# Performance work log

Hardware: AMD Instinct MI355X
Metric: run time of the kernel (lower is better)

Reference implementation:

```python
import jax, jax.numpy as jnp
import numpy as np

K = 16          # nsample
EPS = 1e-5      # BatchNorm eps
NEG_SLOPE = 0.1 # LeakyReLU slope


def _knn_gather(pc2, pc1, feat2, k):
    """pc2 [B,N2,3], pc1 [B,N1,3], feat2 [B,N2,C] ->
       neighbor_xyz [B,N1,k,3], neighbor_feat [B,N1,k,C] (k nearest in pc2 per pc1 point)."""
    # squared euclidean distances (monotone in cdist, same topk indices)
    d2 = (jnp.sum(pc1 * pc1, -1)[:, :, None]
          - 2.0 * jnp.einsum('bic,bjc->bij', pc1, pc2)
          + jnp.sum(pc2 * pc2, -1)[:, None, :])
    idx = jax.lax.top_k(-d2, k)[1]            # [B,N1,k] smallest distances
    gather = jax.vmap(lambda pts, i: pts[i])  # batch-wise fancy gather
    return gather(pc2, idx), gather(feat2, idx)


def _weightnet(xyz, W1, b1, gamma, beta, mean, var, W2, b2):
    """xyz [B,N,K,3] -> [B,N,K,C_out]; Conv2d(1x1)->BN(eval)->ReLU->Conv2d(1x1)."""
    h = jnp.einsum('bnkc,oc->bnko', xyz, W1) + b1
    h = gamma * (h - mean) * jax.lax.rsqrt(var + EPS) + beta
    h = jax.nn.relu(h)
    return jnp.einsum('bnkc,oc->bnko', h, W2) + b2


def _correlator(pc1, pc2, feature1, feature2, mlp_params, wn1, wn2):
    pc1_t = pc1.transpose(0, 2, 1)   # [B,N,3]
    pc2_t = pc2.transpose(0, 2, 1)
    f1 = feature1.transpose(0, 2, 1) # [B,N,C]
    f2 = feature2.transpose(0, 2, 1)
    # Stage 1: point-to-patch cost volume
    nbr_xyz, nbr_f2 = _knn_gather(pc2_t, pc1_t, f2, K)
    direction = nbr_xyz - pc1_t[:, :, None, :]                     # [B,N,K,3]
    f1e = jnp.broadcast_to(f1[:, :, None, :], nbr_f2.shape[:3] + (f1.shape[-1],))
    x = jnp.concatenate([f1e, nbr_f2, direction], axis=-1)         # [B,N,K,2C+3]
    for W, b in mlp_params:
        x = jax.nn.leaky_relu(jnp.einsum('bnkc,oc->bnko', x, W) + b, NEG_SLOPE)
    w1 = _weightnet(direction, *wn1)
    x = jnp.sum(w1 * x, axis=2)                                    # [B,N,C]
    # Stage 2: patch-to-patch self aggregation in pc1 space
    nbr_xyz2, nbr_self = _knn_gather(pc1_t, pc1_t, x, K)
    direction2 = nbr_xyz2 - pc1_t[:, :, None, :]
    w2 = _weightnet(direction2, *wn2)
    out = jnp.sum(w2 * nbr_self, axis=2)                           # [B,N,C]
    return out.transpose(0, 2, 1)                                  # [B,C,N]


def setup_inputs() -> dict:
    key = jax.random.key(0)
    ks = jax.random.split(key, 24)
    B, N, C = 2, 4096, 256
    inc = 2 * C + 3  # 515
    nrm = lambda k, s, sc: (jax.random.normal(k, s, dtype=jnp.float32) * sc)
    uni = lambda k, s: jax.random.uniform(k, s, dtype=jnp.float32, minval=0.5, maxval=1.5)
    return {
        'pc1': nrm(ks[0], (B, 3, N), 1.0),
        'pc2': nrm(ks[1], (B, 3, N), 1.0),
        'feature1': nrm(ks[2], (B, C, N), 1.0),
        'feature2': nrm(ks[3], (B, C, N), 1.0),
        # MLP 1x1 conv stack
        'W0': nrm(ks[4], (C, inc), 0.05), 'b0': jnp.zeros((C,), jnp.float32),
        'W1': nrm(ks[5], (C, C), 0.05),  'b1': jnp.zeros((C,), jnp.float32),
        'W2': nrm(ks[6], (C, C), 0.05),  'b2': jnp.zeros((C,), jnp.float32),
        # WeightNet 1 (3->8->C)
        'wn1_W1': nrm(ks[7], (8, 3), 0.5), 'wn1_b1': jnp.zeros((8,), jnp.float32),
        'wn1_gamma': uni(ks[8], (8,)), 'wn1_beta': nrm(ks[9], (8,), 0.1),
        'wn1_mean': nrm(ks[10], (8,), 0.1), 'wn1_var': uni(ks[11], (8,)),
        'wn1_W2': nrm(ks[12], (C, 8), 0.1), 'wn1_b2': jnp.zeros((C,), jnp.float32),
        # WeightNet 2
        'wn2_W1': nrm(ks[13], (8, 3), 0.5), 'wn2_b1': jnp.zeros((8,), jnp.float32),
        'wn2_gamma': uni(ks[14], (8,)), 'wn2_beta': nrm(ks[15], (8,), 0.1),
        'wn2_mean': nrm(ks[16], (8,), 0.1), 'wn2_var': uni(ks[17], (8,)),
        'wn2_W2': nrm(ks[18], (C, 8), 0.1), 'wn2_b2': jnp.zeros((C,), jnp.float32),
    }


def reference(pc1, pc2, feature1, feature2,
              W0, b0, W1, b1, W2, b2,
              wn1_W1, wn1_b1, wn1_gamma, wn1_beta, wn1_mean, wn1_var, wn1_W2, wn1_b2,
              wn2_W1, wn2_b1, wn2_gamma, wn2_beta, wn2_mean, wn2_var, wn2_W2, wn2_b2):
    mlp_params = [(W0, b0), (W1, b1), (W2, b2)]
    wn1 = (wn1_W1, wn1_b1, wn1_gamma, wn1_beta, wn1_mean, wn1_var, wn1_W2, wn1_b2)
    wn2 = (wn2_W1, wn2_b1, wn2_gamma, wn2_beta, wn2_mean, wn2_var, wn2_W2, wn2_b2)
    return _correlator(pc1, pc2, feature1, feature2, mlp_params, wn1, wn2)
```

## Files before the change

### kernel.cpp

```cpp
#include <hip/hip_runtime.h>
#include <math.h>

#define KNB 16
#define NPTS 4096
#define NB 2
#define CH 256
#define BNEPS 1e-5f

#define MTOT (NB * NPTS * KNB)
#define BM 128

typedef short bf16x8 __attribute__((ext_vector_type(8)));
typedef float f32x4 __attribute__((ext_vector_type(4)));

__device__ __forceinline__ unsigned short f2bf(float x) {
  unsigned u = __float_as_uint(x);
  return (unsigned short)((u + 0x7fffu + ((u >> 16) & 1u)) >> 16);
}
__device__ __forceinline__ float bf2f(unsigned short h) {
  return __uint_as_float(((unsigned)h) << 16);
}

#define GLOAD_LDS16(g, l)                                                     \
  __builtin_amdgcn_global_load_lds(                                           \
      (const __attribute__((address_space(1))) unsigned int*)(g),             \
      (__attribute__((address_space(3))) unsigned int*)(l), 16, 0, 0)

__global__ __launch_bounds__(256) void pack2_pts(const float* __restrict__ pc1,
                                                 const float* __restrict__ pc2,
                                                 float4* __restrict__ pk1,
                                                 float4* __restrict__ pk2) {
  int id = blockIdx.x * 256 + threadIdx.x;
  const float* in = (id < 8192) ? pc1 : pc2;
  float4* out = (id < 8192) ? pk1 : pk2;
  int q = id & 8191;
  int b = q >> 12, n = q & 4095;
  const float* pb = in + (size_t)b * 3 * NPTS;
  float x = pb[n], y = pb[NPTS + n], z = pb[2 * NPTS + n];
  float nn = __fadd_rn(__fadd_rn(__fmul_rn(x, x), __fmul_rn(y, y)), __fmul_rn(z, z));
  out[q] = make_float4(x, y, z, nn);
}

__global__ __launch_bounds__(256) void knn3c_kernel(const float4* __restrict__ pk1,
                                                    const float4* __restrict__ pk2,
                                                    int* __restrict__ idx1,
                                                    int* __restrict__ idx2) {
  __shared__ unsigned short sarr[4][4096];
  __shared__ unsigned long long surv[4][128];
  const int wid = threadIdx.x >> 6;
  const int lane = threadIdx.x & 63;
  const int gw = blockIdx.x * 4 + wid;
  const int which = gw >> 13;
  const int qi = gw & 8191;
  const int b = qi >> 12;
  const float4* pts = (which ? pk1 : pk2) + ((size_t)b << 12);
  float4 qp = pk1[qi];
  const float qx = qp.x, qy = qp.y, qz = qp.z, qn = qp.w;
  unsigned short* S = sarr[wid];

  unsigned int mymin = 0xFFFFu;
#pragma unroll 8
  for (int it = 0; it < 64; ++it) {
    int j = (it << 6) + lane;
    float4 pt = pts[j];
    float dot = __fadd_rn(__fadd_rn(__fmul_rn(qx, pt.x), __fmul_rn(qy, pt.y)),
                          __fmul_rn(qz, pt.z));
    float d = __fadd_rn(__fsub_rn(qn, __fmul_rn(2.f, dot)), pt.w);
    unsigned int u = __float_as_uint(d);
    unsigned int s = u ^ (unsigned int)(((int)u >> 31) | (int)0x80000000);
    unsigned int k16 = s >> 16;
    S[j] = (unsigned short)k16;
    mymin = mymin < k16 ? mymin : k16;
  }

  unsigned int v = mymin;
#pragma unroll
  for (int k = 2; k <= 64; k <<= 1) {
#pragma unroll
    for (int jj = k >> 1; jj >= 1; jj >>= 1) {
      unsigned int o = (unsigned int)__shfl_xor((int)v, jj);
      bool up = ((lane & k) == 0);
      bool low = ((lane & jj) == 0);
      bool tmin = (up == low);
      unsigned int mn = v < o ? v : o;
      unsigned int mx = v < o ? o : v;
      v = tmin ? mn : mx;
    }
  }

  unsigned long long* SV = surv[wid];
  unsigned int thr = (unsigned int)__shfl((int)v, 15);
  int base = 0;
  for (int attempt = 0; attempt < 2; ++attempt) {
    SV[lane] = ~0ull;
    SV[64 + lane] = ~0ull;
    base = 0;
    for (int it = 0; it < 64; ++it) {
      int j = (it << 6) + lane;
      bool hit = (unsigned int)S[j] <= thr;
      unsigned long long m = __ballot(hit);
      if (m) {
        float4 pt = pts[j];
        float dot = __fadd_rn(__fadd_rn(__fmul_rn(qx, pt.x), __fmul_rn(qy, pt.y)),
                              __fmul_rn(qz, pt.z));
        float d = __fadd_rn(__fsub_rn(qn, __fmul_rn(2.f, dot)), pt.w);
        unsigned int u = __float_as_uint(d);
        unsigned int s = u ^ (unsigned int)(((int)u >> 31) | (int)0x80000000);
        int r = base + (int)__popcll(m & ((1ull << lane) - 1ull));
        if (hit && r < 128) SV[r] = ((unsigned long long)s << 32) | (unsigned int)j;
        base += (int)__popcll(m);
      }
    }
    if (base <= 128) break;
    if (attempt == 0) {
      int idx = 23, cnt = 0, tries = 0;
      for (;;) {
        thr = (unsigned int)__shfl((int)v, idx);
        cnt = 0;
        for (int it = 0; it < 64; ++it) {
          unsigned long long m = __ballot((unsigned int)S[(it << 6) + lane] <= thr);
          cnt += __popcll(m);
        }
        if ((cnt >= 16 && cnt <= 128) || ++tries >= 6) break;
        if (cnt < 16) idx = (idx + 12 > 63) ? 63 : idx + 12;
        else idx = (idx - 8 < 0) ? 0 : idx - 8;
      }
    }
  }
  unsigned long long k0 = SV[lane];
  unsigned long long k1 = SV[64 + lane];

#pragma unroll
  for (int k = 2; k <= 128; k <<= 1) {
#pragma unroll
    for (int jj = k >> 1; jj >= 1; jj >>= 1) {
      if (jj == 64) {
        unsigned long long a = k0 < k1 ? k0 : k1;
        unsigned long long c = k0 < k1 ? k1 : k0;
        k0 = a; k1 = c;
      } else {
        {
          unsigned long long o = __shfl_xor(k0, jj);
          bool up = ((lane & k) == 0);
          bool low = ((lane & jj) == 0);
          bool tmin = (up == low);
          unsigned long long mn = k0 < o ? k0 : o;
          unsigned long long mx = k0 < o ? o : k0;
          k0 = tmin ? mn : mx;
        }
        {
          unsigned long long o = __shfl_xor(k1, jj);
          int e = 64 + lane;
          bool up = ((e & k) == 0);
          bool low = ((lane & jj) == 0);
          bool tmin = (up == low);
          unsigned long long mn = k1 < o ? k1 : o;
          unsigned long long mx = k1 < o ? o : k1;
          k1 = tmin ? mn : mx;
        }
      }
    }
  }

  int* op = (which ? idx2 : idx1) + (size_t)qi * KNB;
  if (lane < 16) op[lane] = (int)(k0 & 0xFFFFFFFFu);
}

__global__ __launch_bounds__(256) void conv_feat2(const float* __restrict__ f1,
                                                  const float* __restrict__ f2,
                                                  unsigned short* __restrict__ f1b,
                                                  unsigned short* __restrict__ f2b) {
  int gid = blockIdx.x;
  const float* in = (gid < 8192) ? f1 : f2;
  unsigned short* out = (gid < 8192) ? f1b : f2b;
  int bn = gid & 8191;
  int b = bn >> 12, n = bn & 4095;
  int c = threadIdx.x;
  out[(size_t)bn * CH + c] = f2bf(in[((size_t)(b * CH + c)) * NPTS + n]);
}

__global__ __launch_bounds__(256) void conv_w2(const float* __restrict__ W0,
                                               const float* __restrict__ W1,
                                               const float* __restrict__ W2,
                                               unsigned short* __restrict__ W0a,
                                               unsigned short* __restrict__ W0bp,
                                               unsigned short* __restrict__ W1b,
                                               unsigned short* __restrict__ W2b) {
  int r = blockIdx.x, c = threadIdx.x;
  if (r < 256) {
    W0a[r * 256 + c] = f2bf(W0[(size_t)r * 515 + c]);
    W0bp[r * 256 + c] = f2bf(W0[(size_t)r * 515 + 256 + c]);
  } else if (r < 512) {
    int rr = r - 256;
    W1b[rr * 256 + c] = f2bf(W1[rr * 256 + c]);
  } else {
    int rr = r - 512;
    W2b[rr * 256 + c] = f2bf(W2[rr * 256 + c]);
  }
}

__global__ __launch_bounds__(512) void small_gemm(
    const unsigned short* __restrict__ f1b, const unsigned short* __restrict__ f2b,
    const unsigned short* __restrict__ W0a, const unsigned short* __restrict__ W0bp,
    const float* __restrict__ b0, float* __restrict__ g1, float* __restrict__ G2) {
  __shared__ char smem[8192 + 16384];
  const int tid = threadIdx.x;
  const int lane = tid & 63;
  const int w = tid >> 6;
  const int wm = w >> 2, wn = w & 3;
  const bool isG2 = blockIdx.x >= 64;
  const int m0 = (blockIdx.x & 63) * BM;
  const unsigned short* Asrc = isG2 ? f2b : f1b;
  const unsigned short* Wb = isG2 ? W0bp : W0a;
  float* dst = isG2 ? G2 : g1;

  f32x4 acc[4][4];
#pragma unroll
  for (int nf = 0; nf < 4; ++nf) {
    float bv = isG2 ? 0.f : b0[wn * 64 + nf * 16 + (lane & 15)];
#pragma unroll
    for (int mf = 0; mf < 4; ++mf) acc[mf][nf] = (f32x4){bv, bv, bv, bv};
  }

  const int ar = tid >> 2;
  const int aql = (tid & 3) ^ ((ar >> 1) & 3);
  const int am = m0 + ar;
  const int br0 = tid >> 2;
  const int bq0 = (tid & 3) ^ ((br0 >> 1) & 3);
  const int br1 = (tid + 512) >> 2;
  const int bq1 = (tid & 3) ^ ((br1 >> 1) & 3);

  char* AsW = smem + (w << 10);
  char* BsW0 = smem + 8192 + (w << 10);
  char* BsW1 = smem + 8192 + 8192 + (w << 10);

  for (int kc = 0; kc < 8; ++kc) {
    __syncthreads();
    GLOAD_LDS16(Asrc + ((size_t)am << 8) + kc * 32 + aql * 8, AsW);
    GLOAD_LDS16(Wb + (size_t)br0 * 256 + kc * 32 + bq0 * 8, BsW0);
    GLOAD_LDS16(Wb + (size_t)br1 * 256 + kc * 32 + bq1 * 8, BsW1);
    __syncthreads();

    bf16x8 af[4], bfr[4];
#pragma unroll
    for (int mf = 0; mf < 4; ++mf) {
      int r = wm * 64 + mf * 16 + (lane & 15);
      int off = r * 64 + ((((lane >> 4)) ^ ((r >> 1) & 3)) << 4);
      af[mf] = *(const bf16x8*)(smem + off);
    }
#pragma unroll
    for (int nf = 0; nf < 4; ++nf) {
      int r = wn * 64 + nf * 16 + (lane & 15);
      int off = r * 64 + ((((lane >> 4)) ^ ((r >> 1) & 3)) << 4);
      bfr[nf] = *(const bf16x8*)(smem + 8192 + off);
    }
#pragma unroll
    for (int mf = 0; mf < 4; ++mf)
#pragma unroll
      for (int nf = 0; nf < 4; ++nf)
        acc[mf][nf] = __builtin_amdgcn_mfma_f32_16x16x32_bf16(af[mf], bfr[nf], acc[mf][nf], 0, 0, 0);
  }

#pragma unroll
  for (int mf = 0; mf < 4; ++mf) {
#pragma unroll
    for (int nf = 0; nf < 4; ++nf) {
      int n = wn * 64 + nf * 16 + (lane & 15);
#pragma unroll
      for (int j = 0; j < 4; ++j) {
        int m = m0 + wm * 64 + mf * 16 + (lane >> 4) * 4 + j;
        dst[(size_t)m * 256 + n] = acc[mf][nf][j];
      }
    }
  }
}

__global__ __launch_bounds__(256) void combine_kernel(
    const float* __restrict__ g1, const float* __restrict__ G2,
    const float* __restrict__ W0,
    const float* __restrict__ pc1, const float* __restrict__ pc2,
    const int* __restrict__ idx1,
    const float* __restrict__ wW1, const float* __restrict__ wb1,
    const float* __restrict__ wg, const float* __restrict__ wbe,
    const float* __restrict__ wmn, const float* __restrict__ wv,
    unsigned short* __restrict__ h1, float* __restrict__ h1wn) {
  __shared__ int nbrs[KNB];
  __shared__ float dirs[KNB][4];
  int bn = blockIdx.x;
  int b = bn >> 12, n = bn & 4095;
  int t = threadIdx.x;
  if (t < KNB) nbrs[t] = idx1[(size_t)bn * KNB + t];
  __syncthreads();
  if (t < 128) {
    int k = t >> 3, jj = t & 7;
    int j = nbrs[k];
    const float* p1 = pc1 + (size_t)b * 3 * NPTS;
    const float* p2 = pc2 + (size_t)b * 3 * NPTS;
    float d0 = p2[j] - p1[n];
    float d1 = p2[NPTS + j] - p1[NPTS + n];
    float d2 = p2[2 * NPTS + j] - p1[2 * NPTS + n];
    if (jj == 0) { dirs[k][0] = d0; dirs[k][1] = d1; dirs[k][2] = d2; }
    float hv = wb1[jj];
    hv = fmaf(d0, wW1[jj * 3], hv);
    hv = fmaf(d1, wW1[jj * 3 + 1], hv);
    hv = fmaf(d2, wW1[jj * 3 + 2], hv);
    hv = wg[jj] * (hv - wmn[jj]) * (1.f / sqrtf(wv[jj] + BNEPS)) + wbe[jj];
    h1wn[(size_t)(bn * KNB + k) * 8 + jj] = fmaxf(hv, 0.f);
  }
  __syncthreads();
  int c = t;
  float g1v = g1[((size_t)bn << 8) + c];
  float wc0 = W0[(size_t)c * 515 + 512];
  float wc1 = W0[(size_t)c * 515 + 513];
  float wc2 = W0[(size_t)c * 515 + 514];
  const float* G2b = G2 + (((size_t)b << 12) << 8);
  unsigned short* hp = h1 + ((size_t)bn * KNB) * 256 + c;
#pragma unroll
  for (int k = 0; k < KNB; ++k) {
    float s = g1v + G2b[((size_t)nbrs[k] << 8) + c];
    s = fmaf(dirs[k][0], wc0, s);
    s = fmaf(dirs[k][1], wc1, s);
    s = fmaf(dirs[k][2], wc2, s);
    s = s >= 0.f ? s : 0.1f * s;
    hp[k * 256] = f2bf(s);
  }
}

__global__ __launch_bounds__(512) void gemm256(
    const unsigned short* __restrict__ Asrc, const unsigned short* __restrict__ Wb,
    const float* __restrict__ bias, unsigned short* __restrict__ dst) {
  __shared__ char smem[8192 + 16384];
  const int tid = threadIdx.x;
  const int lane = tid & 63;
  const int w = tid >> 6;
  const int wm = w >> 2, wn = w & 3;
  const int m0 = blockIdx.x * BM;

  f32x4 acc[4][4];
#pragma unroll
  for (int nf = 0; nf < 4; ++nf) {
    float bv = bias[wn * 64 + nf * 16 + (lane & 15)];
#pragma unroll
    for (int mf = 0; mf < 4; ++mf) acc[mf][nf] = (f32x4){bv, bv, bv, bv};
  }

  const int ar = tid >> 2;
  const int aql = (tid & 3) ^ ((ar >> 1) & 3);
  const int am = m0 + ar;
  const int br0 = tid >> 2;
  const int bq0 = (tid & 3) ^ ((br0 >> 1) & 3);
  const int br1 = (tid + 512) >> 2;
  const int bq1 = (tid & 3) ^ ((br1 >> 1) & 3);

  char* AsW = smem + (w << 10);
  char* BsW0 = smem + 8192 + (w << 10);
  char* BsW1 = smem + 8192 + 8192 + (w << 10);

  for (int kc = 0; kc < 8; ++kc) {
    __syncthreads();
    GLOAD_LDS16(Asrc + ((size_t)am << 8) + kc * 32 + aql * 8, AsW);
    GLOAD_LDS16(Wb + (size_t)br0 * 256 + kc * 32 + bq0 * 8, BsW0);
    GLOAD_LDS16(Wb + (size_t)br1 * 256 + kc * 32 + bq1 * 8, BsW1);
    __syncthreads();

    bf16x8 af[4], bfr[4];
#pragma unroll
    for (int mf = 0; mf < 4; ++mf) {
      int r = wm * 64 + mf * 16 + (lane & 15);
      int off = r * 64 + ((((lane >> 4)) ^ ((r >> 1) & 3)) << 4);
      af[mf] = *(const bf16x8*)(smem + off);
    }
#pragma unroll
    for (int nf = 0; nf < 4; ++nf) {
      int r = wn * 64 + nf * 16 + (lane & 15);
      int off = r * 64 + ((((lane >> 4)) ^ ((r >> 1) & 3)) << 4);
      bfr[nf] = *(const bf16x8*)(smem + 8192 + off);
    }
#pragma unroll
    for (int mf = 0; mf < 4; ++mf)
#pragma unroll
      for (int nf = 0; nf < 4; ++nf)
        acc[mf][nf] = __builtin_amdgcn_mfma_f32_16x16x32_bf16(af[mf], bfr[nf], acc[mf][nf], 0, 0, 0);
  }

#pragma unroll
  for (int mf = 0; mf < 4; ++mf) {
#pragma unroll
    for (int nf = 0; nf < 4; ++nf) {
      int n = wn * 64 + nf * 16 + (lane & 15);
#pragma unroll
      for (int j = 0; j < 4; ++j) {
        int m = m0 + wm * 64 + mf * 16 + (lane >> 4) * 4 + j;
        float v = acc[mf][nf][j];
        v = v >= 0.f ? v : 0.1f * v;
        dst[(size_t)m * 256 + n] = f2bf(v);
      }
    }
  }
}

__global__ __launch_bounds__(512) void gemm256_wred(
    const unsigned short* __restrict__ Asrc, const unsigned short* __restrict__ Wb,
    const float* __restrict__ bias, const float* __restrict__ h1wn,
    const float* __restrict__ wW2, const float* __restrict__ wb2,
    float* __restrict__ out1) {
  __shared__ char smem[8192 + 16384];
  __shared__ float hw[1024];
  const int tid = threadIdx.x;
  const int lane = tid & 63;
  const int w = tid >> 6;
  const int wm = w >> 2, wn = w & 3;
  const int m0 = blockIdx.x * BM;

  hw[tid] = h1wn[(size_t)blockIdx.x * 1024 + tid];
  hw[tid + 512] = h1wn[(size_t)blockIdx.x * 1024 + 512 + tid];

  f32x4 acc[4][4];
#pragma unroll
  for (int nf = 0; nf < 4; ++nf) {
    float bv = bias[wn * 64 + nf * 16 + (lane & 15)];
#pragma unroll
    for (int mf = 0; mf < 4; ++mf) acc[mf][nf] = (f32x4){bv, bv, bv, bv};
  }

  const int ar = tid >> 2;
  const int aql = (tid & 3) ^ ((ar >> 1) & 3);
  const int am = m0 + ar;
  const int br0 = tid >> 2;
  const int bq0 = (tid & 3) ^ ((br0 >> 1) & 3);
  const int br1 = (tid + 512) >> 2;
  const int bq1 = (tid & 3) ^ ((br1 >> 1) & 3);

  char* AsW = smem + (w << 10);
  char* BsW0 = smem + 8192 + (w << 10);
  char* BsW1 = smem + 8192 + 8192 + (w << 10);

  for (int kc = 0; kc < 8; ++kc) {
    __syncthreads();
    GLOAD_LDS16(Asrc + ((size_t)am << 8) + kc * 32 + aql * 8, AsW);
    GLOAD_LDS16(Wb + (size_t)br0 * 256 + kc * 32 + bq0 * 8, BsW0);
    GLOAD_LDS16(Wb + (size_t)br1 * 256 + kc * 32 + bq1 * 8, BsW1);
    __syncthreads();

    bf16x8 af[4], bfr[4];
#pragma unroll
    for (int mf = 0; mf < 4; ++mf) {
      int r = wm * 64 + mf * 16 + (lane & 15);
      int off = r * 64 + ((((lane >> 4)) ^ ((r >> 1) & 3)) << 4);
      af[mf] = *(const bf16x8*)(smem + off);
    }
#pragma unroll
    for (int nf = 0; nf < 4; ++nf) {
      int r = wn * 64 + nf * 16 + (lane & 15);
      int off = r * 64 + ((((lane >> 4)) ^ ((r >> 1) & 3)) << 4);
      bfr[nf] = *(const bf16x8*)(smem + 8192 + off);
    }
#pragma unroll
    for (int mf = 0; mf < 4; ++mf)
#pragma unroll
      for (int nf = 0; nf < 4; ++nf)
        acc[mf][nf] = __builtin_amdgcn_mfma_f32_16x16x32_bf16(af[mf], bfr[nf], acc[mf][nf], 0, 0, 0);
  }

#pragma unroll
  for (int nf = 0; nf < 4; ++nf) {
    int n = wn * 64 + nf * 16 + (lane & 15);
    float wbv = wb2[n];
    float wr[8];
#pragma unroll
    for (int jj = 0; jj < 8; ++jj) wr[jj] = wW2[n * 8 + jj];
#pragma unroll
    for (int mf = 0; mf < 4; ++mf) {
      int bnL = wm * 4 + mf;
      float part = 0.f;
#pragma unroll
      for (int j = 0; j < 4; ++j) {
        int k = (lane >> 4) * 4 + j;
        const float4* hp = (const float4*)&hw[(bnL * 16 + k) * 8];
        float4 ha = hp[0], hb = hp[1];
        float w1 = wbv;
        w1 = fmaf(ha.x, wr[0], w1); w1 = fmaf(ha.y, wr[1], w1);
        w1 = fmaf(ha.z, wr[2], w1); w1 = fmaf(ha.w, wr[3], w1);
        w1 = fmaf(hb.x, wr[4], w1); w1 = fmaf(hb.y, wr[5], w1);
        w1 = fmaf(hb.z, wr[6], w1); w1 = fmaf(hb.w, wr[7], w1);
        float v = acc[mf][nf][j];
        v = v >= 0.f ? v : 0.1f * v;
        v = bf2f(f2bf(v));
        part = fmaf(w1, v, part);
      }
      part += __shfl_xor(part, 16);
      part += __shfl_xor(part, 32);
      if (lane < 16)
        out1[(size_t)(blockIdx.x * 8 + bnL) * 256 + n] = part;
    }
  }
}

__global__ __launch_bounds__(256) void stage2_kernel(
    const float* __restrict__ out1, const float* __restrict__ pc1,
    const int* __restrict__ idx2,
    const float* __restrict__ wn_W1, const float* __restrict__ wn_b1,
    const float* __restrict__ wn_g, const float* __restrict__ wn_be,
    const float* __restrict__ wn_m, const float* __restrict__ wn_v,
    const float* __restrict__ wn_W2, const float* __restrict__ wn_b2,
    float* __restrict__ outp) {
  __shared__ float h1[KNB][8];
  __shared__ int nbrs[KNB];
  int bn = blockIdx.x;
  int b = bn >> 12, n = bn & 4095;
  int t = threadIdx.x;
  if (t < KNB) nbrs[t] = idx2[(size_t)bn * KNB + t];
  __syncthreads();
  if (t < 128) {
    int k = t >> 3, jj = t & 7;
    int j = nbrs[k];
    const float* p1 = pc1 + (size_t)b * 3 * NPTS;
    float d0 = p1[j] - p1[n];
    float d1 = p1[NPTS + j] - p1[NPTS + n];
    float d2v = p1[2 * NPTS + j] - p1[2 * NPTS + n];
    float hv = d0 * wn_W1[jj * 3] + d1 * wn_W1[jj * 3 + 1] + d2v * wn_W1[jj * 3 + 2] + wn_b1[jj];
    hv = wn_g[jj] * (hv - wn_m[jj]) * (1.f / sqrtf(wn_v[jj] + BNEPS)) + wn_be[jj];
    h1[k][jj] = fmaxf(hv, 0.f);
  }
  __syncthreads();
  float wrow[8];
#pragma unroll
  for (int jj = 0; jj < 8; ++jj) wrow[jj] = wn_W2[t * 8 + jj];
  float wb = wn_b2[t];
  float outv = 0.f;
#pragma unroll
  for (int k = 0; k < KNB; ++k) {
    float w2 = wb;
#pragma unroll
    for (int jj = 0; jj < 8; ++jj) w2 = fmaf(h1[k][jj], wrow[jj], w2);
    float v = out1[((size_t)(b * NPTS) + nbrs[k]) * CH + t];
    outv = fmaf(w2, v, outv);
  }
  outp[((size_t)(b * CH) + t) * NPTS + n] = outv;
}

extern "C" void kernel_launch(void* const* d_in, const int* in_sizes, int n_in,
                              void* d_out, int out_size, void* d_ws, size_t ws_size,
                              hipStream_t stream) {
  const float* pc1 = (const float*)d_in[0];
  const float* pc2 = (const float*)d_in[1];
  const float* f1 = (const float*)d_in[2];
  const float* f2 = (const float*)d_in[3];
  const float* W0 = (const float*)d_in[4];
  const float* b0 = (const float*)d_in[5];
  const float* W1 = (const float*)d_in[6];
  const float* b1 = (const float*)d_in[7];
  const float* W2 = (const float*)d_in[8];
  const float* b2 = (const float*)d_in[9];
  const float* wn1_W1 = (const float*)d_in[10];
  const float* wn1_b1 = (const float*)d_in[11];
  const float* wn1_g = (const float*)d_in[12];
  const float* wn1_be = (const float*)d_in[13];
  const float* wn1_m = (const float*)d_in[14];
  const float* wn1_v = (const float*)d_in[15];
  const float* wn1_W2 = (const float*)d_in[16];
  const float* wn1_b2 = (const float*)d_in[17];
  const float* wn2_W1 = (const float*)d_in[18];
  const float* wn2_b1 = (const float*)d_in[19];
  const float* wn2_g = (const float*)d_in[20];
  const float* wn2_be = (const float*)d_in[21];
  const float* wn2_m = (const float*)d_in[22];
  const float* wn2_v = (const float*)d_in[23];
  const float* wn2_W2 = (const float*)d_in[24];
  const float* wn2_b2 = (const float*)d_in[25];

  unsigned short* f1b = (unsigned short*)d_ws;
  unsigned short* f2b = f1b + (size_t)NB * NPTS * CH;
  unsigned short* W0a = f2b + (size_t)NB * NPTS * CH;
  unsigned short* W0bp = W0a + (size_t)256 * 256;
  unsigned short* W1b = W0bp + (size_t)256 * 256;
  unsigned short* W2b = W1b + (size_t)256 * 256;
  unsigned short* h = W2b + (size_t)256 * 256;
  float* g1 = (float*)(h + (size_t)MTOT * 256);
  float* G2 = g1 + (size_t)NB * NPTS * CH;
  float* h1wn = G2 + (size_t)NB * NPTS * CH;
  float* out1 = h1wn + (size_t)MTOT * 8;
  int* idx1 = (int*)(out1 + (size_t)NB * NPTS * CH);
  int* idx2 = idx1 + (size_t)MTOT;
  float4* pk1 = (float4*)(idx2 + (size_t)MTOT);
  float4* pk2 = pk1 + (size_t)NB * NPTS;

  pack2_pts<<<NB * NPTS * 2 / 256, 256, 0, stream>>>(pc1, pc2, pk1, pk2);
  knn3c_kernel<<<NB * NPTS * 2 / 4, 256, 0, stream>>>(pk1, pk2, idx1, idx2);
  conv_feat2<<<NB * NPTS * 2, 256, 0, stream>>>(f1, f2, f1b, f2b);
  conv_w2<<<768, 256, 0, stream>>>(W0, W1, W2, W0a, W0bp, W1b, W2b);
  small_gemm<<<128, 512, 0, stream>>>(f1b, f2b, W0a, W0bp, b0, g1, G2);
  combine_kernel<<<NB * NPTS, 256, 0, stream>>>(
      g1, G2, W0, pc1, pc2, idx1, wn1_W1, wn1_b1, wn1_g, wn1_be, wn1_m, wn1_v,
      h, h1wn);
  gemm256<<<MTOT / BM, 512, 0, stream>>>(h, W1b, b1, h);
  gemm256_wred<<<MTOT / BM, 512, 0, stream>>>(h, W2b, b2, h1wn, wn1_W2, wn1_b2, out1);
  stage2_kernel<<<NB * NPTS, 256, 0, stream>>>(
      out1, pc1, idx2, wn2_W1, wn2_b1, wn2_g, wn2_be, wn2_m, wn2_v, wn2_W2, wn2_b2,
      (float*)d_out);
}
```

Measured before the change: 248.5 us.

## Keep full KNN distance keys in registers and compact survivors via prefix scan

The KNN kernel now keeps all 64 per-lane 32-bit sortable distance keys in registers instead of 16-bit truncated keys in LDS. This removes the second pass that reloaded points and recomputed distances for candidates. Survivors are compacted with a per-lane count plus a wave-wide prefix scan instead of per-iteration ballots. The iterative threshold search is replaced by a single fallback to the 8th-smallest lane minimum. That fallback only guarantees 8 candidates, so it risks returning fewer than 16 neighbours in rare dense cases, and the kernel needs more registers per thread.

```diff
diff --git a/kernel.cpp b/kernel.cpp
--- a/kernel.cpp
+++ b/kernel.cpp
@@ -41,11 +41,10 @@
   out[q] = make_float4(x, y, z, nn);
 }
 
-__global__ __launch_bounds__(256) void knn3c_kernel(const float4* __restrict__ pk1,
+__global__ __launch_bounds__(256) void knn3d_kernel(const float4* __restrict__ pk1,
                                                     const float4* __restrict__ pk2,
                                                     int* __restrict__ idx1,
                                                     int* __restrict__ idx2) {
-  __shared__ unsigned short sarr[4][4096];
   __shared__ unsigned long long surv[4][128];
   const int wid = threadIdx.x >> 6;
   const int lane = threadIdx.x & 63;
@@ -56,10 +55,10 @@
   const float4* pts = (which ? pk1 : pk2) + ((size_t)b << 12);
   float4 qp = pk1[qi];
   const float qx = qp.x, qy = qp.y, qz = qp.z, qn = qp.w;
-  unsigned short* S = sarr[wid];
-
-  unsigned int mymin = 0xFFFFu;
-#pragma unroll 8
+
+  unsigned int sreg[64];
+  unsigned int mymin = 0xFFFFFFFFu;
+#pragma unroll
   for (int it = 0; it < 64; ++it) {
     int j = (it << 6) + lane;
     float4 pt = pts[j];
@@ -68,9 +67,8 @@
     float d = __fadd_rn(__fsub_rn(qn, __fmul_rn(2.f, dot)), pt.w);
     unsigned int u = __float_as_uint(d);
     unsigned int s = u ^ (unsigned int)(((int)u >> 31) | (int)0x80000000);
-    unsigned int k16 = s >> 16;
-    S[j] = (unsigned short)k16;
-    mymin = mymin < k16 ? mymin : k16;
+    sreg[it] = s;
+    mymin = mymin < s ? mymin : s;
   }
 
   unsigned int v = mymin;
@@ -90,42 +88,29 @@
 
   unsigned long long* SV = surv[wid];
   unsigned int thr = (unsigned int)__shfl((int)v, 15);
-  int base = 0;
   for (int attempt = 0; attempt < 2; ++attempt) {
+    int cnt = 0;
+#pragma unroll
+    for (int it = 0; it < 64; ++it) cnt += (sreg[it] <= thr) ? 1 : 0;
+    int incl = cnt;
+#pragma unroll
+    for (int off = 1; off < 64; off <<= 1) {
+      int o = __shfl_up(incl, off);
+      if (lane >= off) incl += o;
+    }
+    int total = __shfl(incl, 63);
+    int pos = incl - cnt;
     SV[lane] = ~0ull;
     SV[64 + lane] = ~0ull;
-    base = 0;
+#pragma unroll
     for (int it = 0; it < 64; ++it) {
-      int j = (it << 6) + lane;
-      bool hit = (unsigned int)S[j] <= thr;
-      unsigned long long m = __ballot(hit);
-      if (m) {
-        float4 pt = pts[j];
-        float dot = __fadd_rn(__fadd_rn(__fmul_rn(qx, pt.x), __fmul_rn(qy, pt.y)),
-                              __fmul_rn(qz, pt.z));
-        float d = __fadd_rn(__fsub_rn(qn, __fmul_rn(2.f, dot)), pt.w);
-        unsigned int u = __float_as_uint(d);
-        unsigned int s = u ^ (unsigned int)(((int)u >> 31) | (int)0x80000000);
-        int r = base + (int)__popcll(m & ((1ull << lane) - 1ull));
-        if (hit && r < 128) SV[r] = ((unsigned long long)s << 32) | (unsigned int)j;
-        base += (int)__popcll(m);
-      }
-    }
-    if (base <= 128) break;
-    if (attempt == 0) {
-      int idx = 23, cnt = 0, tries = 0;
-      for (;;) {
-        thr = (unsigned int)__shfl((int)v, idx);
-        cnt = 0;
-        for (int it = 0; it < 64; ++it) {
-          unsigned long long m = __ballot((unsigned int)S[(it << 6) + lane] <= thr);
-          cnt += __popcll(m);
-        }
-        if ((cnt >= 16 && cnt <= 128) || ++tries >= 6) break;
-        if (cnt < 16) idx = (idx + 12 > 63) ? 63 : idx + 12;
-        else idx = (idx - 8 < 0) ? 0 : idx - 8;
-      }
-    }
+      bool hit = sreg[it] <= thr;
+      if (hit && pos < 128)
+        SV[pos] = ((unsigned long long)sreg[it] << 32) | (unsigned int)((it << 6) + lane);
+      pos += hit ? 1 : 0;
+    }
+    if (total <= 128) break;
+    thr = (unsigned int)__shfl((int)v, 7);
   }
   unsigned long long k0 = SV[lane];
   unsigned long long k1 = SV[64 + lane];
@@ -586,7 +571,7 @@
   float4* pk2 = pk1 + (size_t)NB * NPTS;
 
   pack2_pts<<<NB * NPTS * 2 / 256, 256, 0, stream>>>(pc1, pc2, pk1, pk2);
-  knn3c_kernel<<<NB * NPTS * 2 / 4, 256, 0, stream>>>(pk1, pk2, idx1, idx2);
+  knn3d_kernel<<<NB * NPTS * 2 / 4, 256, 0, stream>>>(pk1, pk2, idx1, idx2);
   conv_feat2<<<NB * NPTS * 2, 256, 0, stream>>>(f1, f2, f1b, f2b);
   conv_w2<<<768, 256, 0, stream>>>(W0, W1, W2, W0a, W0bp, W1b, W2b);
   small_gemm<<<128, 512, 0, stream>>>(f1b, f2b, W0a, W0bp, b0, g1, G2);
```

Result: slower. 274.5 us (+10.5%).
